# Performance work log

Measured on AMD Instinct MI355X. Metric: run time of the kernel, lower is better.

## Reference

```python
import jax, jax.numpy as jnp
import numpy as np

B, H, S, D = 4, 16, 2048, 64

def setup_inputs() -> dict:
    key = jax.random.key(0)
    kq, kk, kv = jax.random.split(key, 3)
    return {
        "query": jax.random.normal(kq, (B, H, S, D), dtype=jnp.float32),
        "key": jax.random.normal(kk, (B, H, S, D), dtype=jnp.float32),
        "value": jax.random.normal(kv, (B, H, S, D), dtype=jnp.float32),
        "dropout_p": 0,
    }

def reference(query, key, value, dropout_p):
    # qk: [B,H,S,S] materialized as in the original (unfused SDPA)
    scale = query.shape[-1] ** -0.5
    qk = jnp.einsum("bhqd,bhkd->bhqk", query, key) * scale
    attn = jax.nn.softmax(qk, axis=-1)
    # dropout_p == 0 -> identity (keeps reference deterministic)
    out = jnp.einsum("bhqk,bhkd->bhqd", attn, value)
    return out
```

## Files before the change

### kernel.cpp

```cpp
#include <hip/hip_runtime.h>
#include <hip/hip_bf16.h>

#define B_   4
#define H_   16
#define SEQ  2048
#define DH   64
#define BM   128
#define BN   64
#define NBH  (B_ * H_)
#define NELEM (NBH * SEQ * DH)

typedef __bf16 bf16x8 __attribute__((ext_vector_type(8)));
typedef float  f32x4  __attribute__((ext_vector_type(4)));
typedef unsigned short u16x8 __attribute__((ext_vector_type(8)));
typedef unsigned short u16x4 __attribute__((ext_vector_type(4)));

__device__ __forceinline__ unsigned short f2bu(float x) {
    __hip_bfloat16 h = __float2bfloat16(x);
    return __builtin_bit_cast(unsigned short, h);
}

__device__ __forceinline__ void ld_lds16(const unsigned short* g, unsigned short* l) {
    __builtin_amdgcn_global_load_lds(
        (const __attribute__((address_space(1))) unsigned int*)(g),
        (__attribute__((address_space(3))) unsigned int*)(l), 16, 0, 0);
}

__global__ __launch_bounds__(256)
void prep_kv(const float* __restrict__ K, const float* __restrict__ V,
             unsigned short* __restrict__ Kb, unsigned short* __restrict__ Vt) {
    __shared__ unsigned short tile[64 * 72];
    const int bh = blockIdx.y;
    const int s0 = blockIdx.x * 64;
    const int t  = threadIdx.x;

    {
        const float* Ki = K + (size_t)bh * SEQ * DH + (size_t)s0 * DH;
        unsigned short* Ko = Kb + (size_t)bh * SEQ * DH + (size_t)s0 * DH;
        for (int jj = 0; jj < 2; ++jj) {
            const int e = (jj * 256 + t) * 8;
            const float4 a = *reinterpret_cast<const float4*>(Ki + e);
            const float4 b = *reinterpret_cast<const float4*>(Ki + e + 4);
            u16x8 u;
            u[0] = f2bu(a.x); u[1] = f2bu(a.y); u[2] = f2bu(a.z); u[3] = f2bu(a.w);
            u[4] = f2bu(b.x); u[5] = f2bu(b.y); u[6] = f2bu(b.z); u[7] = f2bu(b.w);
            *reinterpret_cast<u16x8*>(Ko + e) = u;
        }
    }

    const float* Vb = V + (size_t)bh * SEQ * DH + (size_t)s0 * DH;
    unsigned short* Vo = Vt + (size_t)bh * DH * SEQ;
    {
        const int sl = t >> 2, d0 = (t & 3) * 16;
        for (int c = 0; c < 4; ++c) {
            const float4 v = *reinterpret_cast<const float4*>(Vb + sl * DH + d0 + c * 4);
            u16x4 u; u[0] = f2bu(v.x); u[1] = f2bu(v.y); u[2] = f2bu(v.z); u[3] = f2bu(v.w);
            *reinterpret_cast<u16x4*>(&tile[sl * 72 + d0 + c * 4]) = u;
        }
    }
    __syncthreads();
    {
        const int d = t >> 2, sc0 = (t & 3) * 16;
        for (int c = 0; c < 2; ++c) {
            const int s = sc0 + c * 8;
            u16x8 u;
#pragma unroll
            for (int r = 0; r < 8; ++r) u[r] = tile[(s + r) * 72 + d];
            *reinterpret_cast<u16x8*>(Vo + (size_t)d * SEQ + s0 + s) = u;
        }
    }
}

__global__ __launch_bounds__(256, 4)
void fa_fwd(const float* __restrict__ Qg, const unsigned short* __restrict__ Kb,
            const unsigned short* __restrict__ Vtb, float* __restrict__ Og)
{
    __shared__ __attribute__((aligned(16))) unsigned short smem[16384];

    const int tid  = threadIdx.x;
    const int lane = tid & 63;
    const int wave = tid >> 6;
    const int l15  = lane & 15;
    const int quad = lane >> 4;

    const int bid   = blockIdx.x;
    const int xcd   = bid & 7;
    const int jj    = bid >> 3;
    const int bh    = (xcd << 3) | (jj >> 4);
    const int qtile = jj & 15;

    const float*          Qb  = Qg  + (size_t)bh * SEQ * DH;
    const unsigned short* Kbh = Kb  + (size_t)bh * SEQ * DH;
    const unsigned short* Vbh = Vtb + (size_t)bh * DH * SEQ;
    float*                Ob  = Og  + (size_t)bh * SEQ * DH;

    const int qrow0 = qtile * BM + wave * 32;

    const float CS = 0.125f * 1.4426950408889634f;

    bf16x8 Qf[2][2];
    for (int rt = 0; rt < 2; ++rt) {
        const float* qsrc = Qb + (size_t)(qrow0 + rt * 16 + l15) * DH + quad * 8;
        for (int kt = 0; kt < 2; ++kt) {
            const float4 a = *reinterpret_cast<const float4*>(qsrc + kt * 32);
            const float4 b = *reinterpret_cast<const float4*>(qsrc + kt * 32 + 4);
            union { bf16x8 v; unsigned short u[8]; } tmp;
            tmp.u[0] = f2bu(a.x * CS); tmp.u[1] = f2bu(a.y * CS);
            tmp.u[2] = f2bu(a.z * CS); tmp.u[3] = f2bu(a.w * CS);
            tmp.u[4] = f2bu(b.x * CS); tmp.u[5] = f2bu(b.y * CS);
            tmp.u[6] = f2bu(b.z * CS); tmp.u[7] = f2bu(b.w * CS);
            Qf[rt][kt] = tmp.v;
        }
    }

    bf16x8 ones;
    {
        union { bf16x8 v; unsigned short u[8]; } t;
        for (int i = 0; i < 8; ++i) t.u[i] = 0x3F80;
        ones = t.v;
    }
    const f32x4 fzero = {0.f, 0.f, 0.f, 0.f};

    f32x4 Oacc[2][4];
    f32x4 Lacc[2];
    for (int rt = 0; rt < 2; ++rt) {
        Lacc[rt] = fzero;
        for (int dt = 0; dt < 4; ++dt) Oacc[rt][dt] = fzero;
    }

    const unsigned short* kp[2];
    const unsigned short* vp[2];
    int koff_st[2], voff_st[2];
    for (int i = 0; i < 2; ++i) {
        const int beta = i * 256 + tid;
        {
            const int s    = beta >> 3;
            const int b    = beta & 7;
            const int gnat = b ^ (s & 7);
            const int grow = 32 * (s >> 5) + 8 * ((s >> 2) & 3)
                           + 4 * ((s >> 4) & 1) + (s & 3);
            kp[i]  = Kbh + (size_t)grow * DH + gnat * 8;
        }
        {
            const int d = beta >> 3;
            const int g = (beta & 7) ^ (d & 7);
            vp[i]  = Vbh + (size_t)d * SEQ + g * 8;
        }
        koff_st[i] = (i * 256 + wave * 64) * 8;
        voff_st[i] = 4096 + (i * 256 + wave * 64) * 8;
    }

    const int sx   = l15 & 7;
    const int krd0 = l15 * 64 + ((quad    ) ^ sx) * 8;
    const int krd1 = l15 * 64 + ((quad + 4) ^ sx) * 8;
    const int vrd0 = l15 * 64 + ((quad    ) ^ sx) * 8;
    const int vrd1 = l15 * 64 + ((quad + 4) ^ sx) * 8;

#define STAGE(BUF) do {                                                        \
        _Pragma("unroll")                                                      \
        for (int i = 0; i < 2; ++i) {                                          \
            ld_lds16(kp[i], smem + (BUF) * 8192 + koff_st[i]);                 \
            kp[i] += BN * DH;                                                  \
        }                                                                      \
        _Pragma("unroll")                                                      \
        for (int i = 0; i < 2; ++i) {                                          \
            ld_lds16(vp[i], smem + (BUF) * 8192 + voff_st[i]);                 \
            vp[i] += BN;                                                       \
        }                                                                      \
    } while (0)

#define QK_PAIR(BUF, NT0, SACC) do {                                           \
        _Pragma("unroll")                                                      \
        for (int m = 0; m < 2; ++m) {                                          \
            const bf16x8 kf0 = *reinterpret_cast<const bf16x8*>(               \
                &smem[(BUF) * 8192 + ((NT0) + m) * 1024 + krd0]);              \
            const bf16x8 kf1 = *reinterpret_cast<const bf16x8*>(               \
                &smem[(BUF) * 8192 + ((NT0) + m) * 1024 + krd1]);              \
            SACC[0][m] = __builtin_amdgcn_mfma_f32_16x16x32_bf16(kf0, Qf[0][0], fzero,       0, 0, 0); \
            SACC[0][m] = __builtin_amdgcn_mfma_f32_16x16x32_bf16(kf1, Qf[0][1], SACC[0][m], 0, 0, 0); \
            SACC[1][m] = __builtin_amdgcn_mfma_f32_16x16x32_bf16(kf0, Qf[1][0], fzero,       0, 0, 0); \
            SACC[1][m] = __builtin_amdgcn_mfma_f32_16x16x32_bf16(kf1, Qf[1][1], SACC[1][m], 0, 0, 0); \
        }                                                                      \
    } while (0)

#define LOAD_BFR(BUF, DST, VRD) do {                                           \
        _Pragma("unroll")                                                      \
        for (int dt = 0; dt < 4; ++dt)                                         \
            DST[dt] = *reinterpret_cast<const bf16x8*>(                        \
                &smem[(BUF) * 8192 + 4096 + dt * 1024 + (VRD)]);               \
    } while (0)

#define SM_HALF(SACC, KS) do {                                                 \
        _Pragma("unroll")                                                      \
        for (int rt = 0; rt < 2; ++rt) {                                       \
            union { bf16x8 v; unsigned w[4]; } a;                              \
            _Pragma("unroll")                                                  \
            for (int m = 0; m < 2; ++m) {                                      \
                _Pragma("unroll")                                              \
                for (int rp = 0; rp < 2; ++rp) {                               \
                    const float p0 = __builtin_amdgcn_exp2f(SACC[rt][m][2 * rp    ]); \
                    const float p1 = __builtin_amdgcn_exp2f(SACC[rt][m][2 * rp + 1]); \
                    const unsigned u0 = __builtin_bit_cast(unsigned, p0) + 0x8000u; \
                    const unsigned u1 = __builtin_bit_cast(unsigned, p1) + 0x8000u; \
                    a.w[m * 2 + rp] = __builtin_amdgcn_perm(u1, u0, 0x07060302u); \
                }                                                              \
            }                                                                  \
            af[rt][KS] = a.v;                                                  \
            Lacc[rt] = __builtin_amdgcn_mfma_f32_16x16x32_bf16(a.v, ones, Lacc[rt], 0, 0, 0); \
        }                                                                      \
    } while (0)

#define PV_HALF(KS, BFR) do {                                                  \
        _Pragma("unroll")                                                      \
        for (int dt = 0; dt < 4; ++dt) {                                       \
            Oacc[0][dt] = __builtin_amdgcn_mfma_f32_16x16x32_bf16(af[0][KS], BFR[dt], Oacc[0][dt], 0, 0, 0); \
            Oacc[1][dt] = __builtin_amdgcn_mfma_f32_16x16x32_bf16(af[1][KS], BFR[dt], Oacc[1][dt], 0, 0, 0); \
        }                                                                      \
    } while (0)

#define COMPUTE(BUF) do {                                                      \
        f32x4 SA[2][2], SB[2][2];                                              \
        bf16x8 bfr0[4], bfr1[4];                                               \
        bf16x8 af[2][2];                                                       \
                                        \
        LOAD_BFR(BUF, bfr0, vrd0);                                             \
        __builtin_amdgcn_s_setprio(1);                                         \
        QK_PAIR(BUF, 0, SA);                                                   \
        __builtin_amdgcn_s_setprio(0);                                         \
                                       \
        QK_PAIR(BUF, 2, SB);                                                   \
        SM_HALF(SA, 0);                                                        \
                        \
        LOAD_BFR(BUF, bfr1, vrd1);                                             \
        SM_HALF(SB, 1);                                                        \
        PV_HALF(0, bfr0);                                                      \
                                             \
        __builtin_amdgcn_s_setprio(1);                                         \
        PV_HALF(1, bfr1);                                                      \
        __builtin_amdgcn_s_setprio(0);                                         \
    } while (0)

    STAGE(0);
    __syncthreads();

#pragma unroll 1
    for (int it2 = 0; it2 < 15; ++it2) {
        STAGE(1);
        COMPUTE(0);
        __syncthreads();
        STAGE(0);
        COMPUTE(1);
        __syncthreads();
    }
    STAGE(1);
    COMPUTE(0);
    __syncthreads();
    COMPUTE(1);

#undef STAGE
#undef QK_PAIR
#undef LOAD_BFR
#undef SM_HALF
#undef PV_HALF
#undef COMPUTE

    for (int rt = 0; rt < 2; ++rt) {
        for (int r = 0; r < 4; ++r) {
            const float inv = 1.0f / Lacc[rt][r];
            const int row = qrow0 + rt * 16 + quad * 4 + r;
            float* orow = Ob + (size_t)row * DH + l15;
            for (int dt = 0; dt < 4; ++dt)
                orow[dt * 16] = Oacc[rt][dt][r] * inv;
        }
    }
}

extern "C" void kernel_launch(void* const* d_in, const int* in_sizes, int n_in,
                              void* d_out, int out_size, void* d_ws, size_t ws_size,
                              hipStream_t stream) {
    const float* Q = (const float*)d_in[0];
    const float* K = (const float*)d_in[1];
    const float* V = (const float*)d_in[2];
    float* O = (float*)d_out;

    unsigned short* Kb = (unsigned short*)d_ws;
    unsigned short* Vt = Kb + (size_t)NELEM;

    prep_kv<<<dim3(SEQ / 64, NBH), 256, 0, stream>>>(K, V, Kb, Vt);
    fa_fwd<<<dim3((SEQ / BM) * NBH), dim3(256), 0, stream>>>(Q, Kb, Vt, O);
}
```

Baseline: 224.8 us.

## Double query rows per wave to reuse K/V LDS fragments across more rows

Raises the query tile from 128 to 256 rows per block, so each wave handles 64 rows (four 16-row tiles) instead of 32. Each K and V fragment read from LDS now feeds twice as many MFMAs, and each staged K/V tile is shared by more query rows. The block-to-(bh, qtile) mapping and launch bounds (occupancy 4 to 2) change to match. The compute schedule is also reordered, with V fragments loaded inline per dt rather than prefetched. The cost is much higher register pressure and half as many blocks (512), which can lower occupancy and latency hiding.

```diff
diff --git a/kernel.cpp b/kernel.cpp
--- a/kernel.cpp
+++ b/kernel.cpp
@@ -5,7 +5,7 @@
 #define H_   16
 #define SEQ  2048
 #define DH   64
-#define BM   128
+#define BM   256
 #define BN   64
 #define NBH  (B_ * H_)
 #define NELEM (NBH * SEQ * DH)
@@ -71,7 +71,7 @@
     }
 }
 
-__global__ __launch_bounds__(256, 4)
+__global__ __launch_bounds__(256, 2)
 void fa_fwd(const float* __restrict__ Qg, const unsigned short* __restrict__ Kb,
             const unsigned short* __restrict__ Vtb, float* __restrict__ Og)
 {
@@ -86,21 +86,23 @@
     const int bid   = blockIdx.x;
     const int xcd   = bid & 7;
     const int jj    = bid >> 3;
-    const int bh    = (xcd << 3) | (jj >> 4);
-    const int qtile = jj & 15;
+    const int bh    = (xcd << 3) | (jj >> 3);
+    const int qtile = jj & 7;
 
     const float*          Qb  = Qg  + (size_t)bh * SEQ * DH;
     const unsigned short* Kbh = Kb  + (size_t)bh * SEQ * DH;
     const unsigned short* Vbh = Vtb + (size_t)bh * DH * SEQ;
     float*                Ob  = Og  + (size_t)bh * SEQ * DH;
 
-    const int qrow0 = qtile * BM + wave * 32;
+    const int qrow0 = qtile * BM + wave * 64;
 
     const float CS = 0.125f * 1.4426950408889634f;
 
-    bf16x8 Qf[2][2];
-    for (int rt = 0; rt < 2; ++rt) {
+    bf16x8 Qf[4][2];
+#pragma unroll
+    for (int rt = 0; rt < 4; ++rt) {
         const float* qsrc = Qb + (size_t)(qrow0 + rt * 16 + l15) * DH + quad * 8;
+#pragma unroll
         for (int kt = 0; kt < 2; ++kt) {
             const float4 a = *reinterpret_cast<const float4*>(qsrc + kt * 32);
             const float4 b = *reinterpret_cast<const float4*>(qsrc + kt * 32 + 4);
@@ -121,10 +123,12 @@
     }
     const f32x4 fzero = {0.f, 0.f, 0.f, 0.f};
 
-    f32x4 Oacc[2][4];
-    f32x4 Lacc[2];
-    for (int rt = 0; rt < 2; ++rt) {
+    f32x4 Oacc[4][4];
+    f32x4 Lacc[4];
+#pragma unroll
+    for (int rt = 0; rt < 4; ++rt) {
         Lacc[rt] = fzero;
+#pragma unroll
         for (int dt = 0; dt < 4; ++dt) Oacc[rt][dt] = fzero;
     }
 
@@ -176,23 +180,17 @@
                 &smem[(BUF) * 8192 + ((NT0) + m) * 1024 + krd0]);              \
             const bf16x8 kf1 = *reinterpret_cast<const bf16x8*>(               \
                 &smem[(BUF) * 8192 + ((NT0) + m) * 1024 + krd1]);              \
-            SACC[0][m] = __builtin_amdgcn_mfma_f32_16x16x32_bf16(kf0, Qf[0][0], fzero,       0, 0, 0); \
-            SACC[0][m] = __builtin_amdgcn_mfma_f32_16x16x32_bf16(kf1, Qf[0][1], SACC[0][m], 0, 0, 0); \
-            SACC[1][m] = __builtin_amdgcn_mfma_f32_16x16x32_bf16(kf0, Qf[1][0], fzero,       0, 0, 0); \
-            SACC[1][m] = __builtin_amdgcn_mfma_f32_16x16x32_bf16(kf1, Qf[1][1], SACC[1][m], 0, 0, 0); \
-        }                                                                      \
-    } while (0)
-
-#define LOAD_BFR(BUF, DST, VRD) do {                                           \
-        _Pragma("unroll")                                                      \
-        for (int dt = 0; dt < 4; ++dt)                                         \
-            DST[dt] = *reinterpret_cast<const bf16x8*>(                        \
-                &smem[(BUF) * 8192 + 4096 + dt * 1024 + (VRD)]);               \
+            _Pragma("unroll")                                                  \
+            for (int rt = 0; rt < 4; ++rt) {                                   \
+                SACC[rt][m] = __builtin_amdgcn_mfma_f32_16x16x32_bf16(kf0, Qf[rt][0], fzero,       0, 0, 0); \
+                SACC[rt][m] = __builtin_amdgcn_mfma_f32_16x16x32_bf16(kf1, Qf[rt][1], SACC[rt][m], 0, 0, 0); \
+            }                                                                  \
+        }                                                                      \
     } while (0)
 
 #define SM_HALF(SACC, KS) do {                                                 \
         _Pragma("unroll")                                                      \
-        for (int rt = 0; rt < 2; ++rt) {                                       \
+        for (int rt = 0; rt < 4; ++rt) {                                       \
             union { bf16x8 v; unsigned w[4]; } a;                              \
             _Pragma("unroll")                                                  \
             for (int m = 0; m < 2; ++m) {                                      \
@@ -210,33 +208,31 @@
         }                                                                      \
     } while (0)
 
-#define PV_HALF(KS, BFR) do {                                                  \
+#define PV_HALF(BUF, KS, VRD) do {                                             \
         _Pragma("unroll")                                                      \
         for (int dt = 0; dt < 4; ++dt) {                                       \
-            Oacc[0][dt] = __builtin_amdgcn_mfma_f32_16x16x32_bf16(af[0][KS], BFR[dt], Oacc[0][dt], 0, 0, 0); \
-            Oacc[1][dt] = __builtin_amdgcn_mfma_f32_16x16x32_bf16(af[1][KS], BFR[dt], Oacc[1][dt], 0, 0, 0); \
+            const bf16x8 bfr = *reinterpret_cast<const bf16x8*>(               \
+                &smem[(BUF) * 8192 + 4096 + dt * 1024 + (VRD)]);               \
+            _Pragma("unroll")                                                  \
+            for (int rt = 0; rt < 4; ++rt)                                     \
+                Oacc[rt][dt] = __builtin_amdgcn_mfma_f32_16x16x32_bf16(af[rt][KS], bfr, Oacc[rt][dt], 0, 0, 0); \
         }                                                                      \
     } while (0)
 
 #define COMPUTE(BUF) do {                                                      \
-        f32x4 SA[2][2], SB[2][2];                                              \
-        bf16x8 bfr0[4], bfr1[4];                                               \
-        bf16x8 af[2][2];                                                       \
-                                        \
-        LOAD_BFR(BUF, bfr0, vrd0);                                             \
+        f32x4 SA[4][2], SB[4][2];                                              \
+        bf16x8 af[4][2];                                                       \
         __builtin_amdgcn_s_setprio(1);                                         \
         QK_PAIR(BUF, 0, SA);                                                   \
         __builtin_amdgcn_s_setprio(0);                                         \
-                                       \
+        SM_HALF(SA, 0);              \
+        __builtin_amdgcn_s_setprio(1);                                         \
         QK_PAIR(BUF, 2, SB);                                                   \
-        SM_HALF(SA, 0);                                                        \
-                        \
-        LOAD_BFR(BUF, bfr1, vrd1);                                             \
+        __builtin_amdgcn_s_setprio(0);                                         \
         SM_HALF(SB, 1);                                                        \
-        PV_HALF(0, bfr0);                                                      \
-                                             \
         __builtin_amdgcn_s_setprio(1);                                         \
-        PV_HALF(1, bfr1);                                                      \
+        PV_HALF(BUF, 0, vrd0);                                                 \
+        PV_HALF(BUF, 1, vrd1);                                                 \
         __builtin_amdgcn_s_setprio(0);                                         \
     } while (0)
 
@@ -259,16 +255,18 @@
 
 #undef STAGE
 #undef QK_PAIR
-#undef LOAD_BFR
 #undef SM_HALF
 #undef PV_HALF
 #undef COMPUTE
 
-    for (int rt = 0; rt < 2; ++rt) {
+#pragma unroll
+    for (int rt = 0; rt < 4; ++rt) {
+#pragma unroll
         for (int r = 0; r < 4; ++r) {
             const float inv = 1.0f / Lacc[rt][r];
             const int row = qrow0 + rt * 16 + quad * 4 + r;
             float* orow = Ob + (size_t)row * DH + l15;
+#pragma unroll
             for (int dt = 0; dt < 4; ++dt)
                 orow[dt * 16] = Oacc[rt][dt][r] * inv;
         }
```

After: 199.3 us. 11.4% less time.
